# Kernel tuning notes

Measured on AMD Instinct MI355X. Metric: run time of the kernel, lower is better.

The kernel has to match this reference:

```python
import jax, jax.numpy as jnp
import numpy as np

HEADS = 1
EPS = 1e-12  # torch F.normalize eps


def dwt_haar(x):
    # Haar analysis, J=1, zero mode (even H,W -> no padding needed).
    b, c, H, W = x.shape
    xr = x.reshape(b, c, H // 2, 2, W // 2, 2)
    a = xr[:, :, :, 0, :, 0]
    bb = xr[:, :, :, 0, :, 1]
    cc = xr[:, :, :, 1, :, 0]
    d = xr[:, :, :, 1, :, 1]
    ll = (a + bb + cc + d) * 0.5
    h1 = (a - bb + cc - d) * 0.5  # high in width
    h2 = (a + bb - cc - d) * 0.5  # high in height
    h3 = (a - bb - cc + d) * 0.5  # diagonal
    return ll, h1, h2, h3


def idwt_haar(ll, h1, h2, h3):
    a = (ll + h1 + h2 + h3) * 0.5
    bb = (ll - h1 + h2 - h3) * 0.5
    cc = (ll + h1 - h2 - h3) * 0.5
    d = (ll - h1 - h2 + h3) * 0.5
    row0 = jnp.stack([a, bb], axis=-1)   # (b,c,h2,w2,2)
    row1 = jnp.stack([cc, d], axis=-1)
    y = jnp.stack([row0, row1], axis=3)  # (b,c,h2,2,w2,2)
    b_, c_, h2_, _, w2_, _ = y.shape
    return y.reshape(b_, c_, h2_ * 2, w2_ * 2)


def conv1x1(x, w, bias):
    # x: (b,c,h,w); w: (o,c); bias: (o,)
    return jnp.einsum('oc,bchw->bohw', w, x) + bias[None, :, None, None]


def mdta(x, qw, qb, kw, kb, vw, vb, pw, pb, temp):
    b, c, h, w = x.shape
    q = conv1x1(x, qw, qb).reshape(b, HEADS, c // HEADS, h * w)
    k = conv1x1(x, kw, kb).reshape(b, HEADS, c // HEADS, h * w)
    v = conv1x1(x, vw, vb).reshape(b, HEADS, c // HEADS, h * w)
    q = q / jnp.maximum(jnp.linalg.norm(q, axis=-1, keepdims=True), EPS)
    k = k / jnp.maximum(jnp.linalg.norm(k, axis=-1, keepdims=True), EPS)
    attn = jnp.einsum('bhcn,bhdn->bhcd', q, k) * temp[None]
    attn = jax.nn.softmax(attn, axis=-1)
    out = jnp.einsum('bhcd,bhdn->bhcn', attn, v).reshape(b, c, h, w)
    return conv1x1(out, pw, pb)


def setup_inputs() -> dict:
    key = jax.random.key(0)
    ks = jax.random.split(key, 20)
    B, C, H, W = 16, 64, 256, 256
    C3 = 3 * C
    s1 = 1.0 / np.sqrt(C)
    s3 = 1.0 / np.sqrt(C3)
    d = {'img': jax.random.normal(ks[0], (B, C, H, W), jnp.float32)}
    names = ['qw', 'qb', 'kw', 'kb', 'vw', 'vb', 'pw', 'pb']
    for i, n in enumerate(names):
        if n.endswith('w'):
            d['ll_' + n] = jax.random.normal(ks[1 + i], (C, C), jnp.float32) * s1
            d['h_' + n] = jax.random.normal(ks[10 + i], (C3, C3), jnp.float32) * s3
        else:
            d['ll_' + n] = jax.random.normal(ks[1 + i], (C,), jnp.float32) * s1
            d['h_' + n] = jax.random.normal(ks[10 + i], (C3,), jnp.float32) * s3
    d['ll_temp'] = jnp.ones((HEADS, 1, 1), jnp.float32)
    d['h_temp'] = jnp.ones((HEADS, 1, 1), jnp.float32)
    return d


def reference(img, ll_qw, ll_qb, ll_kw, ll_kb, ll_vw, ll_vb, ll_pw, ll_pb, ll_temp,
              h_qw, h_qb, h_kw, h_kb, h_vw, h_vb, h_pw, h_pb, h_temp):
    b, c, H, W = img.shape
    ll, h1, h2, h3 = dwt_haar(img)
    # rearrange 'b c fp h w -> b (c fp) h w' with fp=3 (bands interleaved per channel)
    hh = jnp.stack([h1, h2, h3], axis=2).reshape(b, c * 3, H // 2, W // 2)
    ll = mdta(ll, ll_qw, ll_qb, ll_kw, ll_kb, ll_vw, ll_vb, ll_pw, ll_pb, ll_temp)
    hh = mdta(hh, h_qw, h_qb, h_kw, h_kb, h_vw, h_vb, h_pw, h_pb, h_temp)
    hh = hh.reshape(b, c, 3, H // 2, W // 2)
    return idwt_haar(ll, hh[:, :, 0], hh[:, :, 1], hh[:, :, 2])
```

## Files before the change

kernel.cpp:

```cpp
#include <hip/hip_runtime.h>

typedef __bf16 bf16;
typedef bf16 bf16x8 __attribute__((ext_vector_type(8)));
typedef bf16 bf16x4 __attribute__((ext_vector_type(4)));
typedef float f32x4 __attribute__((ext_vector_type(4)));

#define NB 16
#define CLL 64
#define CHH 192
#define NPIX 16384
#define SL (CLL * CLL)
#define SH (CHH * CHH)

__global__ __launch_bounds__(256) void k_dwt(const float* __restrict__ img, bf16* __restrict__ xll,
                      bf16* __restrict__ xhh, float* __restrict__ sll, float* __restrict__ shh) {
    int bc = blockIdx.y;
    int b = bc >> 6, c = bc & 63;
    int t = threadIdx.x;
    int r = blockIdx.x * 16 + (t >> 4);
    int q = t & 15;
    const float* p0 = img + ((size_t)bc << 16) + (size_t)(2 * r) * 256 + 16 * q;
    const float* p1 = p0 + 256;
    float4 e0[4], e1[4];
    #pragma unroll
    for (int l = 0; l < 4; l++) { e0[l] = ((const float4*)p0)[l]; e1[l] = ((const float4*)p1)[l]; }
    const float* f0 = (const float*)e0;
    const float* f1 = (const float*)e1;
    bf16x8 vll, v1, v2, v3;
    float s0 = 0.f, s1 = 0.f, s2 = 0.f, s3 = 0.f;
    #pragma unroll
    for (int p = 0; p < 8; p++) {
        float a = f0[2 * p], bb = f0[2 * p + 1], cc = f1[2 * p], d = f1[2 * p + 1];
        float wll = (a + bb + cc + d) * 0.5f;
        float w1  = (a - bb + cc - d) * 0.5f;
        float w2  = (a + bb - cc - d) * 0.5f;
        float w3  = (a - bb - cc + d) * 0.5f;
        vll[p] = (bf16)wll; v1[p] = (bf16)w1; v2[p] = (bf16)w2; v3[p] = (bf16)w3;
        s0 += wll; s1 += w1; s2 += w2; s3 += w3;
    }
    size_t n = (size_t)r * 128 + 8 * q;
    *(bf16x8*)(xll + ((size_t)b * CLL + c) * NPIX + n) = vll;
    size_t hb = ((size_t)b * CHH + 3 * c) * NPIX + n;
    *(bf16x8*)(xhh + hb) = v1;
    *(bf16x8*)(xhh + hb + NPIX) = v2;
    *(bf16x8*)(xhh + hb + 2 * NPIX) = v3;
    for (int o = 32; o; o >>= 1) {
        s0 += __shfl_down(s0, o); s1 += __shfl_down(s1, o);
        s2 += __shfl_down(s2, o); s3 += __shfl_down(s3, o);
    }
    if ((t & 63) == 0) {
        atomicAdd(&sll[b * CLL + c], s0);
        atomicAdd(&shh[b * CHH + 3 * c + 0], s1);
        atomicAdd(&shh[b * CHH + 3 * c + 1], s2);
        atomicAdd(&shh[b * CHH + 3 * c + 2], s3);
    }
}

__global__ __launch_bounds__(256) void k_gramv(const bf16* __restrict__ xll,
        const bf16* __restrict__ xhh, float* __restrict__ Gll, float* __restrict__ Ghh,
        const float* __restrict__ llvw, const float* __restrict__ hvw,
        float* __restrict__ vwTll, float* __restrict__ vwThh) {
    __shared__ bf16 sA[64 * 64];
    __shared__ bf16 sB[64 * 64];
    int blk = blockIdx.x, t = threadIdx.x;
    if (blk >= 1024) {
        int base = (blk - 1024) * 256 + t;
        for (int idx = base; idx < SL + SH; idx += 32 * 256) {
            if (idx < SL) {
                int r = idx / CLL, k = idx % CLL;
                vwTll[idx] = llvw[(size_t)k * CLL + r];
            } else {
                int i2 = idx - SL;
                int r = i2 / CHH, k = i2 % CHH;
                vwThh[i2] = hvw[(size_t)k * CHH + r];
            }
        }
        return;
    }
    int C, ti, tj, sk, b2, KC;
    const bf16* X; float* G;
    if (blk < 768) {
        C = CHH; sk = blk % 8; int tl = (blk / 8) % 6; b2 = blk / 48; KC = 2048;
        ti = (tl < 3) ? 0 : ((tl < 5) ? 1 : 2);
        tj = (tl < 3) ? tl : ((tl < 5) ? tl - 2 : 2);
        X = xhh + (size_t)b2 * CHH * NPIX; G = Ghh + (size_t)b2 * SH;
    } else {
        int j = blk - 768;
        C = CLL; sk = j % 16; b2 = j / 16; KC = 1024; ti = 0; tj = 0;
        X = xll + (size_t)b2 * CLL * NPIX; G = Gll + (size_t)b2 * SL;
    }
    int lane = t & 63, wv = t >> 6;
    int g = lane >> 4, l15 = lane & 15;
    int rowi = t >> 3, chunk = t & 7;
    int k0 = sk * KC;
    const bf16* gA0 = X + (size_t)(ti * 64 + rowi) * NPIX + k0 + chunk * 8;
    const bf16* gA1 = gA0 + (size_t)32 * NPIX;
    const bf16* gB0 = X + (size_t)(tj * 64 + rowi) * NPIX + k0 + chunk * 8;
    const bf16* gB1 = gB0 + (size_t)32 * NPIX;
    int swc = (chunk ^ (rowi & 7)) * 8;
    bf16* lA0 = sA + rowi * 64 + swc;
    bf16* lA1 = sA + (rowi + 32) * 64 + swc;
    bf16* lB0 = sB + rowi * 64 + swc;
    bf16* lB1 = sB + (rowi + 32) * 64 + swc;
    int arow = (wv >> 1) * 32;
    int bcol = (wv & 1) * 32;
    int sw = l15 & 7;
    int roA0 = (arow + l15) * 64, roA1 = roA0 + 16 * 64;
    int roB0 = (bcol + l15) * 64, roB1 = roB0 + 16 * 64;
    f32x4 acc[2][2] = {};
    bf16x8 rA0 = *(const bf16x8*)gA0;
    bf16x8 rA1 = *(const bf16x8*)gA1;
    bf16x8 rB0 = *(const bf16x8*)gB0;
    bf16x8 rB1 = *(const bf16x8*)gB1;
    for (int kc = 0; kc < KC; kc += 64) {
        *(bf16x8*)lA0 = rA0; *(bf16x8*)lA1 = rA1;
        *(bf16x8*)lB0 = rB0; *(bf16x8*)lB1 = rB1;
        __syncthreads();
        if (kc + 64 < KC) {
            rA0 = *(const bf16x8*)(gA0 + kc + 64);
            rA1 = *(const bf16x8*)(gA1 + kc + 64);
            rB0 = *(const bf16x8*)(gB0 + kc + 64);
            rB1 = *(const bf16x8*)(gB1 + kc + 64);
        }
        #pragma unroll
        for (int ks = 0; ks < 2; ks++) {
            int ck = ((ks * 4 + g) ^ sw) * 8;
            bf16x8 a0 = *(const bf16x8*)(sA + roA0 + ck);
            bf16x8 a1 = *(const bf16x8*)(sA + roA1 + ck);
            bf16x8 b0 = *(const bf16x8*)(sB + roB0 + ck);
            bf16x8 b1 = *(const bf16x8*)(sB + roB1 + ck);
            acc[0][0] = __builtin_amdgcn_mfma_f32_16x16x32_bf16(a0, b0, acc[0][0], 0, 0, 0);
            acc[0][1] = __builtin_amdgcn_mfma_f32_16x16x32_bf16(a0, b1, acc[0][1], 0, 0, 0);
            acc[1][0] = __builtin_amdgcn_mfma_f32_16x16x32_bf16(a1, b0, acc[1][0], 0, 0, 0);
            acc[1][1] = __builtin_amdgcn_mfma_f32_16x16x32_bf16(a1, b1, acc[1][1], 0, 0, 0);
        }
        __syncthreads();
    }
    int r0q = ti * 64 + arow;
    int c0q = tj * 64 + bcol;
    bool offd = (ti != tj);
    #pragma unroll
    for (int rr = 0; rr < 2; rr++)
        #pragma unroll
        for (int c2 = 0; c2 < 2; c2++)
            #pragma unroll
            for (int rg = 0; rg < 4; rg++) {
                int row = r0q + rr * 16 + g * 4 + rg;
                int col = c0q + c2 * 16 + l15;
                float v = acc[rr][c2][rg];
                atomicAdd(&G[(size_t)row * C + col], v);
                if (offd) atomicAdd(&G[(size_t)col * C + row], v);
            }
}

template <typename OUT>
__global__ __launch_bounds__(256) void k_ntu(
        const float* __restrict__ Xll0, const float* __restrict__ Xll1, long XllbS,
        const float* __restrict__ Yll, long YllbS,
        OUT* __restrict__ Oll, long OllzS, long OllbS,
        const float* __restrict__ Xhh0, const float* __restrict__ Xhh1, long XhhbS,
        const float* __restrict__ Yhh, long YhhbS,
        OUT* __restrict__ Ohh, long OhhzS, long OhhbS) {
    int x = blockIdx.x, b = blockIdx.y, z = blockIdx.z;
    int C, rt, ct;
    const float *X, *Y;
    OUT* O;
    if (x == 0) {
        C = CLL; rt = 0; ct = 0;
        X = (z ? Xll1 : Xll0) + (size_t)b * XllbS;
        Y = Yll + (size_t)b * YllbS;
        O = Oll + (size_t)z * OllzS + (size_t)b * OllbS;
    } else {
        C = CHH; int tl = x - 1; rt = tl / 3; ct = tl % 3;
        X = (z ? Xhh1 : Xhh0) + (size_t)b * XhhbS;
        Y = Yhh + (size_t)b * YhhbS;
        O = Ohh + (size_t)z * OhhzS + (size_t)b * OhhbS;
    }
    int t = threadIdx.x, ti = t >> 4, tj = t & 15;
    const float* xr = X + (size_t)(rt * 64 + ti * 4) * C;
    const float* yr = Y + (size_t)(ct * 64 + tj * 4) * C;
    float acc[4][4] = {};
    for (int k = 0; k < C; k += 4) {
        float4 xa[4], yb[4];
        #pragma unroll
        for (int a = 0; a < 4; a++) xa[a] = *(const float4*)(xr + (size_t)a * C + k);
        #pragma unroll
        for (int q = 0; q < 4; q++) yb[q] = *(const float4*)(yr + (size_t)q * C + k);
        #pragma unroll
        for (int a = 0; a < 4; a++)
            #pragma unroll
            for (int q = 0; q < 4; q++)
                acc[a][q] += xa[a].x * yb[q].x + xa[a].y * yb[q].y
                           + xa[a].z * yb[q].z + xa[a].w * yb[q].w;
    }
    #pragma unroll
    for (int a = 0; a < 4; a++) {
        int row = rt * 64 + ti * 4 + a, col = ct * 64 + tj * 4;
        if constexpr (sizeof(OUT) == 4) {
            *(float4*)((float*)O + (size_t)row * C + col) =
                make_float4(acc[a][0], acc[a][1], acc[a][2], acc[a][3]);
        } else {
            bf16x4 v;
            v[0] = (bf16)acc[a][0]; v[1] = (bf16)acc[a][1];
            v[2] = (bf16)acc[a][2]; v[3] = (bf16)acc[a][3];
            *(bf16x4*)((bf16*)O + (size_t)row * C + col) = v;
        }
    }
}

__global__ __launch_bounds__(256) void k_lnrm(
        const float* __restrict__ PRll, const float* __restrict__ PRhh,
        const float* __restrict__ llqw, const float* __restrict__ llkw,
        const float* __restrict__ hqw,  const float* __restrict__ hkw,
        const float* __restrict__ llqb, const float* __restrict__ llkb,
        const float* __restrict__ hqb,  const float* __restrict__ hkb,
        const float* __restrict__ sll,  const float* __restrict__ shh,
        float* __restrict__ nrmll, float* __restrict__ nrmhh,
        float* __restrict__ wsll,  float* __restrict__ wshh,
        float* __restrict__ Lll, float* __restrict__ Lhh) {
    int blk = blockIdx.x, t = threadIdx.x;
    int wvv = t >> 6, lane = t & 63;
    for (int wt = blk * 4 + wvv; wt < 8192; wt += 640) {
        int z = wt >> 12, b2 = (wt >> 8) & 15, gr = wt & 255;
        int C, i; const float *P, *w, *wb, *s; float *nrm, *ws;
        if (gr < CLL) {
            C = CLL; i = gr;
            P = PRll + ((size_t)z * NB + b2) * SL;
            w = z ? llkw : llqw; wb = z ? llkb : llqb;
            s = sll + (size_t)b2 * CLL;
            nrm = nrmll + ((size_t)z * NB + b2) * CLL;
            ws  = wsll  + ((size_t)z * NB + b2) * CLL;
        } else {
            C = CHH; i = gr - CLL;
            P = PRhh + ((size_t)z * NB + b2) * SH;
            w = z ? hkw : hqw; wb = z ? hkb : hqb;
            s = shh + (size_t)b2 * CHH;
            nrm = nrmhh + ((size_t)z * NB + b2) * CHH;
            ws  = wshh  + ((size_t)z * NB + b2) * CHH;
        }
        const float* Pi = P + (size_t)i * C;
        const float* wi = w + (size_t)i * C;
        float np = 0.f, sd = 0.f;
        for (int j = lane; j < C; j += 64) {
            float wj = wi[j];
            np += Pi[j] * wj;
            sd += wj * s[j];
        }
        for (int o = 32; o; o >>= 1) { np += __shfl_down(np, o); sd += __shfl_down(sd, o); }
        if (lane == 0) {
            float wbi = wb[i];
            float q2 = np + 2.f * wbi * sd + (float)NPIX * wbi * wbi;
            nrm[i] = fmaxf(sqrtf(fmaxf(q2, 0.f)), 1e-12f);
            ws[i] = sd;
        }
    }
    int x = blk % 10, b = blk / 10;
    int C, rt, ct;
    const float *X, *Y; float* O;
    if (x == 0) {
        C = CLL; rt = 0; ct = 0;
        X = PRll + (size_t)b * SL; Y = llkw; O = Lll + (size_t)b * SL;
    } else {
        C = CHH; int tl = x - 1; rt = tl / 3; ct = tl % 3;
        X = PRhh + (size_t)b * SH; Y = hkw; O = Lhh + (size_t)b * SH;
    }
    int ti = t >> 4, tj = t & 15;
    const float* xr = X + (size_t)(rt * 64 + ti * 4) * C;
    const float* yr = Y + (size_t)(ct * 64 + tj * 4) * C;
    float acc[4][4] = {};
    for (int k = 0; k < C; k += 4) {
        float4 xa[4], yb[4];
        #pragma unroll
        for (int a = 0; a < 4; a++) xa[a] = *(const float4*)(xr + (size_t)a * C + k);
        #pragma unroll
        for (int q = 0; q < 4; q++) yb[q] = *(const float4*)(yr + (size_t)q * C + k);
        #pragma unroll
        for (int a = 0; a < 4; a++)
            #pragma unroll
            for (int q = 0; q < 4; q++)
                acc[a][q] += xa[a].x * yb[q].x + xa[a].y * yb[q].y
                           + xa[a].z * yb[q].z + xa[a].w * yb[q].w;
    }
    #pragma unroll
    for (int a = 0; a < 4; a++) {
        int row = rt * 64 + ti * 4 + a, col = ct * 64 + tj * 4;
        *(float4*)(O + (size_t)row * C + col) =
            make_float4(acc[a][0], acc[a][1], acc[a][2], acc[a][3]);
    }
}

__global__ __launch_bounds__(256) void k_soft2(
        const float* __restrict__ Lll, const float* __restrict__ Lhh,
        const float* __restrict__ llkb, const float* __restrict__ llqb,
        const float* __restrict__ hkb,  const float* __restrict__ hqb,
        const float* __restrict__ nrmll, const float* __restrict__ nrmhh,
        const float* __restrict__ wsll,  const float* __restrict__ wshh,
        const float* __restrict__ llvb,  const float* __restrict__ hvb,
        const float* __restrict__ lltp,  const float* __restrict__ htp,
        float* __restrict__ All, float* __restrict__ Ahh,
        float* __restrict__ avll, float* __restrict__ avhh) {
    int b = blockIdx.y;
    int wv = threadIdx.x >> 6, lane = threadIdx.x & 63;
    int gr = blockIdx.x * 4 + wv;
    int C, i; const float *Lb, *kb, *qb, *qn, *kn, *qs, *ks, *vb, *tp;
    float *A, *av;
    if (gr < CLL) {
        C = CLL; i = gr;
        Lb = Lll + (size_t)b * SL; kb = llkb; qb = llqb;
        qn = nrmll + (size_t)b * CLL;  kn = nrmll + ((size_t)NB + b) * CLL;
        qs = wsll + (size_t)b * CLL;   ks = wsll + ((size_t)NB + b) * CLL;
        vb = llvb; tp = lltp;
        A = All + (size_t)b * SL; av = avll + (size_t)b * CLL;
    } else {
        C = CHH; i = gr - CLL;
        Lb = Lhh + (size_t)b * SH; kb = hkb; qb = hqb;
        qn = nrmhh + (size_t)b * CHH;  kn = nrmhh + ((size_t)NB + b) * CHH;
        qs = wshh + (size_t)b * CHH;   ks = wshh + ((size_t)NB + b) * CHH;
        vb = hvb; tp = htp;
        A = Ahh + (size_t)b * SH; av = avhh + (size_t)b * CHH;
    }
    const float* Li = Lb + (size_t)i * C;
    float qni = qn[i], qsi = qs[i], qbi = qb[i], tmp = tp[0];
    float Lv[3];
    #pragma unroll
    for (int s2 = 0; s2 < 3; s2++) {
        int j = lane + s2 * 64;
        if (j < C) {
            float l = Li[j] + qsi * kb[j] + qbi * ks[j] + (float)NPIX * qbi * kb[j];
            Lv[s2] = l / (qni * kn[j]) * tmp;
        } else Lv[s2] = -1e30f;
    }
    float mx = fmaxf(fmaxf(Lv[0], Lv[1]), Lv[2]);
    for (int o = 32; o; o >>= 1) mx = fmaxf(mx, __shfl_xor(mx, o));
    float e[3], sum = 0.f;
    #pragma unroll
    for (int s2 = 0; s2 < 3; s2++) {
        e[s2] = (lane + s2 * 64 < C) ? expf(Lv[s2] - mx) : 0.f;
        sum += e[s2];
    }
    for (int o = 32; o; o >>= 1) sum += __shfl_xor(sum, o);
    float inv = 1.f / sum;
    float avp = 0.f;
    #pragma unroll
    for (int s2 = 0; s2 < 3; s2++) {
        int j = lane + s2 * 64;
        if (j < C) {
            float a = e[s2] * inv;
            A[(size_t)i * C + j] = a;
            avp += a * vb[j];
        }
    }
    for (int o = 32; o; o >>= 1) avp += __shfl_down(avp, o);
    if (lane == 0) av[i] = avp;
}

__global__ __launch_bounds__(256) void k_wtmv(
        const float* __restrict__ vwTll, const float* __restrict__ vwThh,
        const float* __restrict__ All, const float* __restrict__ Ahh,
        const float* __restrict__ llpw, const float* __restrict__ llpb,
        const float* __restrict__ hpw,  const float* __restrict__ hpb,
        const float* __restrict__ avll, const float* __restrict__ avhh,
        float* __restrict__ WTll, float* __restrict__ WThh,
        float* __restrict__ mvll, float* __restrict__ mvhh) {
    int blk = blockIdx.x, t = threadIdx.x;
    int wvv = t >> 6, lane = t & 63;
    for (int wt = blk * 4 + wvv; wt < 4096; wt += 640) {
        int b2 = wt >> 8, gr = wt & 255;
        int C, i; const float *pw, *pb_, *av_; float* mv_;
        if (gr < CLL) {
            C = CLL; i = gr;
            pw = llpw; pb_ = llpb; av_ = avll + (size_t)b2 * CLL; mv_ = mvll + (size_t)b2 * CLL;
        } else {
            C = CHH; i = gr - CLL;
            pw = hpw; pb_ = hpb; av_ = avhh + (size_t)b2 * CHH; mv_ = mvhh + (size_t)b2 * CHH;
        }
        const float* pwi = pw + (size_t)i * C;
        float m = 0.f;
        for (int k = lane; k < C; k += 64) m += pwi[k] * av_[k];
        for (int o = 32; o; o >>= 1) m += __shfl_down(m, o);
        if (lane == 0) mv_[i] = m + pb_[i];
    }
    int x = blk % 10, b = blk / 10;
    int C, rt, ct;
    const float *X, *Y; float* O;
    if (x == 0) {
        C = CLL; rt = 0; ct = 0;
        X = vwTll; Y = All + (size_t)b * SL; O = WTll + (size_t)b * SL;
    } else {
        C = CHH; int tl = x - 1; rt = tl / 3; ct = tl % 3;
        X = vwThh; Y = Ahh + (size_t)b * SH; O = WThh + (size_t)b * SH;
    }
    int ti = t >> 4, tj = t & 15;
    const float* xr = X + (size_t)(rt * 64 + ti * 4) * C;
    const float* yr = Y + (size_t)(ct * 64 + tj * 4) * C;
    float acc[4][4] = {};
    for (int k = 0; k < C; k += 4) {
        float4 xa[4], yb[4];
        #pragma unroll
        for (int a = 0; a < 4; a++) xa[a] = *(const float4*)(xr + (size_t)a * C + k);
        #pragma unroll
        for (int q = 0; q < 4; q++) yb[q] = *(const float4*)(yr + (size_t)q * C + k);
        #pragma unroll
        for (int a = 0; a < 4; a++)
            #pragma unroll
            for (int q = 0; q < 4; q++)
                acc[a][q] += xa[a].x * yb[q].x + xa[a].y * yb[q].y
                           + xa[a].z * yb[q].z + xa[a].w * yb[q].w;
    }
    #pragma unroll
    for (int a = 0; a < 4; a++) {
        int row = rt * 64 + ti * 4 + a, col = ct * 64 + tj * 4;
        *(float4*)(O + (size_t)row * C + col) =
            make_float4(acc[a][0], acc[a][1], acc[a][2], acc[a][3]);
    }
}

__global__ __launch_bounds__(256) void k_final(const bf16* __restrict__ xll, const bf16* __restrict__ xhh,
                        const bf16* __restrict__ Mll, const bf16* __restrict__ Mhh,
                        const float* __restrict__ mvll, const float* __restrict__ mvhh,
                        float* __restrict__ out) {
    __shared__ alignas(16) float smemf[256 * 65];
    bf16* sxl = (bf16*)smemf;
    bf16* sxh = (bf16*)smemf + 64 * 64;
    float* Y = smemf;
    int b = blockIdx.y, tile = blockIdx.x;
    int irow = tile >> 1, j0 = (tile & 1) << 6;
    int n0 = irow * 128 + j0;
    int t = threadIdx.x;
    const bf16* Xl = xll + (size_t)b * CLL * NPIX;
    const bf16* Xh = xhh + (size_t)b * CHH * NPIX;
    for (int task = t; task < 512; task += 256) {
        int d = task >> 3, q = task & 7;
        bf16x8 v = *(const bf16x8*)(Xl + (size_t)d * NPIX + n0 + q * 8);
        int cs = (((d >> 3) ^ q) << 3) | (d & 7);
        #pragma unroll
        for (int p = 0; p < 8; p++) sxl[(q * 8 + p) * 64 + cs] = v[p];
    }
    for (int task = t; task < 1536; task += 256) {
        int d = task >> 3, q = task & 7;
        bf16x8 v = *(const bf16x8*)(Xh + (size_t)d * NPIX + n0 + q * 8);
        int c = d >> 3;
        int cs = ((((c & ~7) | ((c & 7) ^ q))) << 3) | (d & 7);
        #pragma unroll
        for (int p = 0; p < 8; p++) sxh[(q * 8 + p) * 192 + cs] = v[p];
    }
    __syncthreads();
    int wv = t >> 6, lane = t & 63, g = lane >> 4, l15 = lane & 15;
    f32x4 accL[4] = {};
    {
        const bf16* M = Mll + (size_t)b * SL + (size_t)(wv * 16 + l15) * CLL;
        #pragma unroll
        for (int ks = 0; ks < 2; ks++) {
            bf16x8 af = *(const bf16x8*)(M + ks * 32 + g * 8);
            int cc = ks * 4 + g;
            #pragma unroll
            for (int c2 = 0; c2 < 4; c2++) {
                int pxr = c2 * 16 + l15;
                int csw = cc ^ ((pxr >> 3) & 7);
                bf16x8 bfrag = *(const bf16x8*)(sxl + pxr * 64 + csw * 8);
                accL[c2] = __builtin_amdgcn_mfma_f32_16x16x32_bf16(af, bfrag, accL[c2], 0, 0, 0);
            }
        }
    }
    f32x4 accH[3][4] = {};
    {
        const bf16* M = Mhh + (size_t)b * SH;
        #pragma unroll 2
        for (int kb = 0; kb < CHH; kb += 32) {
            bf16x8 af[3];
            #pragma unroll
            for (int r = 0; r < 3; r++)
                af[r] = *(const bf16x8*)(M + (size_t)(wv * 48 + r * 16 + l15) * CHH + kb + g * 8);
            #pragma unroll
            for (int c2 = 0; c2 < 4; c2++) {
                int pxr = c2 * 16 + l15;
                int cc = (kb >> 3) + g;
                int csw = (cc & ~7) | ((cc & 7) ^ ((pxr >> 3) & 7));
                bf16x8 bfrag = *(const bf16x8*)(sxh + pxr * 192 + csw * 8);
                #pragma unroll
                for (int r = 0; r < 3; r++)
                    accH[r][c2] = __builtin_amdgcn_mfma_f32_16x16x32_bf16(af[r], bfrag, accH[r][c2], 0, 0, 0);
            }
        }
    }
    __syncthreads();
    #pragma unroll
    for (int c2 = 0; c2 < 4; c2++)
        #pragma unroll
        for (int rg = 0; rg < 4; rg++) {
            int rl = wv * 16 + g * 4 + rg;
            Y[rl * 65 + c2 * 16 + l15] = accL[c2][rg] + mvll[b * CLL + rl];
        }
    #pragma unroll
    for (int r = 0; r < 3; r++)
        #pragma unroll
        for (int c2 = 0; c2 < 4; c2++)
            #pragma unroll
            for (int rg = 0; rg < 4; rg++) {
                int rh = wv * 48 + r * 16 + g * 4 + rg;
                Y[(64 + rh) * 65 + c2 * 16 + l15] = accH[r][c2][rg] + mvhh[b * CHH + rh];
            }
    __syncthreads();
    int p = t & 63, cg = t >> 6;
    float* ob = out + ((size_t)b * CLL) * 65536;
    for (int it = 0; it < 16; it++) {
        int c = it * 4 + cg;
        float ll = Y[c * 65 + p];
        float h1 = Y[(64 + 3 * c + 0) * 65 + p];
        float h2 = Y[(64 + 3 * c + 1) * 65 + p];
        float h3 = Y[(64 + 3 * c + 2) * 65 + p];
        float a  = (ll + h1 + h2 + h3) * 0.5f;
        float bb = (ll - h1 + h2 - h3) * 0.5f;
        float cc = (ll + h1 - h2 - h3) * 0.5f;
        float d  = (ll - h1 - h2 + h3) * 0.5f;
        int jj = j0 + p;
        float2* o0 = (float2*)(ob + ((size_t)c * 256 + 2 * irow) * 256 + 2 * jj);
        float2* o1 = (float2*)(ob + ((size_t)c * 256 + 2 * irow + 1) * 256 + 2 * jj);
        *o0 = make_float2(a, bb);
        *o1 = make_float2(cc, d);
    }
}

extern "C" void kernel_launch(void* const* d_in, const int* in_sizes, int n_in,
                              void* d_out, int out_size, void* d_ws, size_t ws_size,
                              hipStream_t stream) {
    const float* img    = (const float*)d_in[0];
    const float* ll_qw = (const float*)d_in[1];  const float* h_qw = (const float*)d_in[2];
    const float* ll_qb = (const float*)d_in[3];  const float* h_qb = (const float*)d_in[4];
    const float* ll_kw = (const float*)d_in[5];  const float* h_kw = (const float*)d_in[6];
    const float* ll_kb = (const float*)d_in[7];  const float* h_kb = (const float*)d_in[8];
    const float* ll_vw = (const float*)d_in[9];  const float* h_vw = (const float*)d_in[10];
    const float* ll_vb = (const float*)d_in[11]; const float* h_vb = (const float*)d_in[12];
    const float* ll_pw = (const float*)d_in[13]; const float* h_pw = (const float*)d_in[14];
    const float* ll_pb = (const float*)d_in[15]; const float* h_pb = (const float*)d_in[16];
    const float* ll_tp = (const float*)d_in[17]; const float* h_tp = (const float*)d_in[18];
    float* out = (float*)d_out;

    char* ws = (char*)d_ws;
    size_t off = 0;
    auto alloc = [&](size_t sz) { char* p = ws + off; off += (sz + 255) & ~(size_t)255; return p; };
    bf16*  xll  = (bf16*) alloc((size_t)NB * CLL * NPIX * 2);
    bf16*  xhh  = (bf16*) alloc((size_t)NB * CHH * NPIX * 2);
    char*  zb   = ws + off;
    float* sll  = (float*)alloc(NB * CLL * 4);
    float* shh  = (float*)alloc(NB * CHH * 4);
    float* Gll  = (float*)alloc((size_t)NB * SL * 4);
    float* Ghh  = (float*)alloc((size_t)NB * SH * 4);
    size_t zsz  = (size_t)((ws + off) - zb);
    float* PRll = (float*)alloc(2 * (size_t)NB * SL * 4);
    float* PRhh = (float*)alloc(2 * (size_t)NB * SH * 4);
    float* nrmll= (float*)alloc(2 * NB * CLL * 4);
    float* nrmhh= (float*)alloc(2 * NB * CHH * 4);
    float* wsll = (float*)alloc(2 * NB * CLL * 4);
    float* wshh = (float*)alloc(2 * NB * CHH * 4);
    float* Lll  = (float*)alloc((size_t)NB * SL * 4);
    float* Lhh  = (float*)alloc((size_t)NB * SH * 4);
    float* All  = (float*)alloc((size_t)NB * SL * 4);
    float* Ahh  = (float*)alloc((size_t)NB * SH * 4);
    float* avll = (float*)alloc(NB * CLL * 4);   float* avhh = (float*)alloc(NB * CHH * 4);
    float* WTll = (float*)alloc((size_t)NB * SL * 4);
    float* WThh = (float*)alloc((size_t)NB * SH * 4);
    float* vwTll= (float*)alloc(SL * 4);
    float* vwThh= (float*)alloc(SH * 4);
    bf16*  Mll  = (bf16*) alloc((size_t)NB * SL * 2);
    bf16*  Mhh  = (bf16*) alloc((size_t)NB * SH * 2);
    float* mvll = (float*)alloc(NB * CLL * 4);   float* mvhh = (float*)alloc(NB * CHH * 4);

    hipMemsetAsync(zb, 0, zsz, stream);

    k_dwt<<<dim3(8, NB * 64), 256, 0, stream>>>(img, xll, xhh, sll, shh);

    k_gramv<<<1056, 256, 0, stream>>>(xll, xhh, Gll, Ghh, ll_vw, h_vw, vwTll, vwThh);

    k_ntu<float><<<dim3(10, NB, 2), 256, 0, stream>>>(
        ll_qw, ll_kw, 0, Gll, (long)SL, PRll, (long)NB * SL, (long)SL,
        h_qw,  h_kw,  0, Ghh, (long)SH, PRhh, (long)NB * SH, (long)SH);

    k_lnrm<<<160, 256, 0, stream>>>(PRll, PRhh,
        ll_qw, ll_kw, h_qw, h_kw, ll_qb, ll_kb, h_qb, h_kb, sll, shh,
        nrmll, nrmhh, wsll, wshh, Lll, Lhh);

    k_soft2<<<dim3(64, NB), 256, 0, stream>>>(Lll, Lhh, ll_kb, ll_qb, h_kb, h_qb,
        nrmll, nrmhh, wsll, wshh, ll_vb, h_vb, ll_tp, h_tp, All, Ahh, avll, avhh);

    k_wtmv<<<160, 256, 0, stream>>>(vwTll, vwThh, All, Ahh,
        ll_pw, ll_pb, h_pw, h_pb, avll, avhh, WTll, WThh, mvll, mvhh);

    k_ntu<bf16><<<dim3(10, NB, 1), 256, 0, stream>>>(
        ll_pw, ll_pw, 0, WTll, (long)SL, Mll, 0, (long)SL,
        h_pw,  h_pw,  0, WThh, (long)SH, Mhh, 0, (long)SH);

    k_final<<<dim3(256, NB), 256, 0, stream>>>(xll, xhh, Mll, Mhh, mvll, mvhh, out);
}
```

Measured before the change: 460.1 us.

## Mirror Gram matrix in a separate pass and split row-reduction work into extra blocks

The Gram kernel now does one atomicAdd per element instead of also writing the mirrored transpose element. A new k_prep2 kernel then copies the upper triangle into the lower triangle. In k_lnrm and k_wtmv, the per-row dot-product loops that were interleaved into 160 blocks now run as separate extra blocks (one wave per row), so they execute in parallel with the tiled GEMM blocks instead of before them. This cuts the atomic traffic in half and improves parallelism, at the cost of an extra kernel launch and an extra pass over the Gram matrices.

```diff
diff --git a/kernel.cpp b/kernel.cpp
--- a/kernel.cpp
+++ b/kernel.cpp
@@ -138,7 +138,6 @@
     }
     int r0q = ti * 64 + arow;
     int c0q = tj * 64 + bcol;
-    bool offd = (ti != tj);
     #pragma unroll
     for (int rr = 0; rr < 2; rr++)
         #pragma unroll
@@ -147,10 +146,25 @@
             for (int rg = 0; rg < 4; rg++) {
                 int row = r0q + rr * 16 + g * 4 + rg;
                 int col = c0q + c2 * 16 + l15;
-                float v = acc[rr][c2][rg];
-                atomicAdd(&G[(size_t)row * C + col], v);
-                if (offd) atomicAdd(&G[(size_t)col * C + row], v);
+                atomicAdd(&G[(size_t)row * C + col], acc[rr][c2][rg]);
             }
+}
+
+__global__ void k_prep2(float* __restrict__ Gll, float* __restrict__ Ghh) {
+    int total = NB * (SL + SH);
+    for (int idx = blockIdx.x * 256 + threadIdx.x; idx < total; idx += gridDim.x * 256) {
+        int b = idx / (SL + SH), r = idx % (SL + SH);
+        if (r < SL) {
+            float* Gb = Gll + (size_t)b * SL;
+            int i = r / CLL, j = r % CLL;
+            if (j < i) Gb[r] = Gb[(size_t)j * CLL + i];
+        } else {
+            int r2 = r - SL;
+            float* Gb = Ghh + (size_t)b * SH;
+            int i = r2 / CHH, j = r2 % CHH;
+            if (j < i) Gb[r2] = Gb[(size_t)j * CHH + i];
+        }
+    }
 }
 
 template <typename OUT>
@@ -219,8 +233,9 @@
         float* __restrict__ wsll,  float* __restrict__ wshh,
         float* __restrict__ Lll, float* __restrict__ Lhh) {
     int blk = blockIdx.x, t = threadIdx.x;
-    int wvv = t >> 6, lane = t & 63;
-    for (int wt = blk * 4 + wvv; wt < 8192; wt += 640) {
+    if (blk >= 160) {
+        int wvv = t >> 6, lane = t & 63;
+        int wt = (blk - 160) * 4 + wvv;
         int z = wt >> 12, b2 = (wt >> 8) & 15, gr = wt & 255;
         int C, i; const float *P, *w, *wb, *s; float *nrm, *ws;
         if (gr < CLL) {
@@ -253,6 +268,7 @@
             nrm[i] = fmaxf(sqrtf(fmaxf(q2, 0.f)), 1e-12f);
             ws[i] = sd;
         }
+        return;
     }
     int x = blk % 10, b = blk / 10;
     int C, rt, ct;
@@ -363,8 +379,9 @@
         float* __restrict__ WTll, float* __restrict__ WThh,
         float* __restrict__ mvll, float* __restrict__ mvhh) {
     int blk = blockIdx.x, t = threadIdx.x;
-    int wvv = t >> 6, lane = t & 63;
-    for (int wt = blk * 4 + wvv; wt < 4096; wt += 640) {
+    if (blk >= 160) {
+        int wvv = t >> 6, lane = t & 63;
+        int wt = (blk - 160) * 4 + wvv;
         int b2 = wt >> 8, gr = wt & 255;
         int C, i; const float *pw, *pb_, *av_; float* mv_;
         if (gr < CLL) {
@@ -379,6 +396,7 @@
         for (int k = lane; k < C; k += 64) m += pwi[k] * av_[k];
         for (int o = 32; o; o >>= 1) m += __shfl_down(m, o);
         if (lane == 0) mv_[i] = m + pb_[i];
+        return;
     }
     int x = blk % 10, b = blk / 10;
     int C, rt, ct;
@@ -572,18 +590,20 @@
 
     k_gramv<<<1056, 256, 0, stream>>>(xll, xhh, Gll, Ghh, ll_vw, h_vw, vwTll, vwThh);
 
+    k_prep2<<<1024, 256, 0, stream>>>(Gll, Ghh);
+
     k_ntu<float><<<dim3(10, NB, 2), 256, 0, stream>>>(
         ll_qw, ll_kw, 0, Gll, (long)SL, PRll, (long)NB * SL, (long)SL,
         h_qw,  h_kw,  0, Ghh, (long)SH, PRhh, (long)NB * SH, (long)SH);
 
-    k_lnrm<<<160, 256, 0, stream>>>(PRll, PRhh,
+    k_lnrm<<<2208, 256, 0, stream>>>(PRll, PRhh,
         ll_qw, ll_kw, h_qw, h_kw, ll_qb, ll_kb, h_qb, h_kb, sll, shh,
         nrmll, nrmhh, wsll, wshh, Lll, Lhh);
 
     k_soft2<<<dim3(64, NB), 256, 0, stream>>>(Lll, Lhh, ll_kb, ll_qb, h_kb, h_qb,
         nrmll, nrmhh, wsll, wshh, ll_vb, h_vb, ll_tp, h_tp, All, Ahh, avll, avhh);
 
-    k_wtmv<<<160, 256, 0, stream>>>(vwTll, vwThh, All, Ahh,
+    k_wtmv<<<1184, 256, 0, stream>>>(vwTll, vwThh, All, Ahh,
         ll_pw, ll_pb, h_pw, h_pb, avll, avhh, WTll, WThh, mvll, mvhh);
 
     k_ntu<bf16><<<dim3(10, NB, 1), 256, 0, stream>>>(
```

New measurement: 417.2 us. 9.3% less time.
